# Kernel tuning notes

Measured on AMD Instinct MI355X. Metric: run time of the kernel, lower is better.

Reference implementation:

```python
import jax, jax.numpy as jnp
import numpy as np

HEADS, DIM_HEAD, BLOCK, EPS = 16, 64, 16, 1e-8


def _hattn(x, w_qkv, w_out, b_out):
    b, n, dim = x.shape
    h, dh, bsz = HEADS, DIM_HEAD, BLOCK
    scale = dh ** -0.5
    # n is a power of two, so the module's pad-to-pow2 step is a no-op.
    qkv = x @ w_qkv  # [b, n, 3*h*dh]
    q, k, v = jnp.split(qkv, 3, axis=-1)

    def to_heads(t):  # [b, n, h*dh] -> [(b h), n, dh]
        return t.reshape(b, n, h, dh).transpose(0, 2, 1, 3).reshape(b * h, n, dh)

    q, k, v = to_heads(q) * scale, to_heads(k), to_heads(v)

    num_levels = int(np.log2(n // bsz)) - 1
    levels = [(q, k, v)]
    for _ in range(num_levels):  # coarsen: mean-pool q,k; sum-pool v (mask=None path)
        q = q.reshape(b * h, -1, 2, dh).mean(axis=2)
        k = k.reshape(b * h, -1, 2, dh).mean(axis=2)
        v = v.reshape(b * h, -1, 2, dh).sum(axis=2)
        levels.append((q, k, v))

    def flip_blocks(t):  # swap adjacent blocks along the block axis: [B, nb, z, d]
        B, nb, z, d = t.shape
        return t.reshape(B, nb // 2, 2, z, d)[:, :, ::-1].reshape(B, nb, z, d)

    Ys = []
    last = len(levels) - 1
    for ind, (ql, kl, vl) in enumerate(reversed(levels)):  # coarsest -> finest
        B, N, d = ql.shape
        qb = ql.reshape(B, N // bsz, bsz, d)
        kb = vb = None
        kb = kl.reshape(B, N // bsz, bsz, d)
        vb = vl.reshape(B, N // bsz, bsz, d)
        if ind != last:  # off-diagonal pairing at coarse levels
            kb, vb = flip_blocks(kb), flip_blocks(vb)
        S = jnp.einsum('bnid,bnjd->bnij', qb, kb)
        S = S - S.max(axis=-1, keepdims=True)
        A = jnp.exp(S)
        y = jnp.einsum('bnij,bnjd->bnid', A, vb)
        Ys.append((y.reshape(B, N, d), A.sum(-1).reshape(B, N)))

    Y, Asum = Ys[0]
    for y_l, a_l in Ys[1:]:  # upsample-and-accumulate across levels
        Y = jnp.repeat(Y, 2, axis=1) + y_l
        Asum = jnp.repeat(Asum, 2, axis=1) + a_l

    out = Y / (Asum + EPS)[..., None]  # [(b h), n, dh]
    out = out.reshape(b, h, n, dh).transpose(0, 2, 1, 3).reshape(b, n, h * dh)
    return out @ w_out + b_out


def setup_inputs() -> dict:
    key = jax.random.key(0)
    k1, k2, k3 = jax.random.split(key, 3)
    b, n, dim = 4, 8192, 1024
    inner = HEADS * DIM_HEAD
    x = jax.random.normal(k1, (b, n, dim), dtype=jnp.float32)
    w_qkv = jax.random.normal(k2, (dim, inner * 3), dtype=jnp.float32) * 0.02
    w_out = jax.random.normal(k3, (inner, dim), dtype=jnp.float32) * 0.02
    b_out = jnp.zeros((dim,), dtype=jnp.float32)
    return {"x": x, "w_qkv": w_qkv, "w_out": w_out, "b_out": b_out}


def reference(x, w_qkv, w_out, b_out):
    return _hattn(x, w_qkv, w_out, b_out)
```

## Files before the change

### kernel.cpp

```cpp
#include <hip/hip_runtime.h>

typedef unsigned short u16;
typedef unsigned int u32;
typedef __bf16 bf16x8 __attribute__((ext_vector_type(8)));
typedef float f32x4 __attribute__((ext_vector_type(4)));

__device__ inline float bf2f(u16 u) { u32 x = ((u32)u) << 16; return __uint_as_float(x); }
__device__ inline u16 f2bf(float f) {
  u32 x = __float_as_uint(f);
  u32 r = (x + 0x7FFFu + ((x >> 16) & 1u)) >> 16;
  return (u16)r;
}
__device__ inline u32 pack2(float lo, float hi) {
  return (u32)f2bf(lo) | ((u32)f2bf(hi) << 16);
}

__global__ __launch_bounds__(256) void cast_bf16(const float* __restrict__ s,
                                                 u16* __restrict__ d, int n4) {
  const float4* s4 = (const float4*)s;
  u32* d2 = (u32*)d;
  int i = blockIdx.x * 256 + threadIdx.x;
  int stride = gridDim.x * 256;
  for (; i < n4; i += stride) {
    float4 f = s4[i];
    d2[2 * i]     = pack2(f.x, f.y);
    d2[2 * i + 1] = pack2(f.z, f.w);
  }
}

__global__ __launch_bounds__(256) void transpose_cast(const float* __restrict__ src,
                                                      u16* __restrict__ dst, int R, int C) {
  __shared__ float tile[32][33];
  int bx = blockIdx.x, by = blockIdx.y;
  int tx = threadIdx.x & 31, ty = threadIdx.x >> 5;
  for (int rr = ty; rr < 32; rr += 8)
    tile[rr][tx] = src[(size_t)(by * 32 + rr) * C + bx * 32 + tx];
  __syncthreads();
  for (int rr = ty; rr < 32; rr += 8)
    dst[(size_t)(bx * 32 + rr) * R + by * 32 + tx] = f2bf(tile[tx][rr]);
}

#define MFMAQ(AF, BF, MO, NO)                                                     \
  _Pragma("unroll") for (int mf = 0; mf < 4; ++mf)                                \
  _Pragma("unroll") for (int nf = 0; nf < 2; ++nf)                                \
  _Pragma("unroll") for (int kq = 0; kq < 2; ++kq)                                \
    acc[(MO) + mf][(NO) + nf] = __builtin_amdgcn_mfma_f32_16x16x32_bf16(          \
        AF[mf][kq], BF[nf][kq], acc[(MO) + mf][(NO) + nf], 0, 0, 0);

#define PH_OPEN12                                                                 \
  asm volatile("s_waitcnt lgkmcnt(8)" ::: "memory");                              \
  __builtin_amdgcn_s_barrier();                                                   \
  asm volatile("s_waitcnt lgkmcnt(0)" ::: "memory");                              \
  __builtin_amdgcn_sched_barrier(0);                                              \
  __builtin_amdgcn_s_setprio(1);

#define PH_OPEN                                                                   \
  __builtin_amdgcn_s_barrier();                                                   \
  asm volatile("s_waitcnt lgkmcnt(0)" ::: "memory");                              \
  __builtin_amdgcn_sched_barrier(0);                                              \
  __builtin_amdgcn_s_setprio(1);

#define PH_CLOSE                                                                  \
  __builtin_amdgcn_s_setprio(0);                                                  \
  __builtin_amdgcn_s_barrier();                                                   \
  __builtin_amdgcn_sched_barrier(0);

#define PH_CLOSE_VM8                                                              \
  __builtin_amdgcn_s_setprio(0);                                                  \
  asm volatile("s_waitcnt vmcnt(8)" ::: "memory");                                \
  __builtin_amdgcn_s_barrier();                                                   \
  __builtin_amdgcn_sched_barrier(0);

template <int EPI>
__global__ __launch_bounds__(512, 2) void gemm8p(
    const u16* __restrict__ A, const u16* __restrict__ Bt, int M, int N, int K, int NB,
    u16* __restrict__ q0, u16* __restrict__ k0, u16* __restrict__ v0,
    u16* __restrict__ q4, u16* __restrict__ k4, u16* __restrict__ v4,
    float* __restrict__ out, const float* __restrict__ bias) {
  __shared__ u16 ldsA[3][16384];
  __shared__ u16 ldsB[2][16384];
  const int tid = threadIdx.x;
  const int lane = tid & 63;
  const int wave = tid >> 6;
  const int wm = wave >> 2, wn = wave & 3;
  const int lr = lane & 15, lg = lane >> 4;

  const int nwg = gridDim.x;
  const int bid = blockIdx.x;
  const int swz = (bid & 7) * (nwg >> 3) + (bid >> 3);
  const int m0 = (swz / NB) * 256;
  const int n0 = (swz % NB) * 256;
  const int NT = K >> 6;

  auto stage_half = [&](u16* ldsop, const u16* src, int r0, int hb, int kt_) {
#pragma unroll
    for (int ii = 0; ii < 2; ++ii) {
      int c2 = (hb * 2 + ii) * 512 + tid;
      int row = c2 >> 3, ps = c2 & 7;
      int ks = ps ^ (row & 7);
      const u16* g = src + (size_t)(r0 + row) * K + kt_ + ks * 8;
      char* l = (char*)ldsop + (size_t)(((hb * 2 + ii) * 512 + (tid & ~63)) * 16);
      __builtin_amdgcn_global_load_lds((const __attribute__((address_space(1))) void*)g,
                                       (__attribute__((address_space(3))) void*)l, 16, 0, 0);
    }
  };
  auto rdA = [&](const u16* Ab, int mf, int kq) -> bf16x8 {
    int rl = wm * 128 + mf * 16 + lr;
    int sl = (kq * 4 + lg) ^ (rl & 7);
    return *(const bf16x8*)(Ab + rl * 64 + sl * 8);
  };
  auto rdB = [&](const u16* Bb, int nf, int kq) -> bf16x8 {
    int rl = wn * 64 + nf * 16 + lr;
    int sl = (kq * 4 + lg) ^ (rl & 7);
    return *(const bf16x8*)(Bb + rl * 64 + sl * 8);
  };

  f32x4 acc[8][4];
#pragma unroll
  for (int mf = 0; mf < 8; ++mf)
#pragma unroll
    for (int nf = 0; nf < 4; ++nf) acc[mf][nf] = f32x4{0.f, 0.f, 0.f, 0.f};

  stage_half(ldsA[0], A, m0, 0, 0); stage_half(ldsA[0], A, m0, 1, 0);
  stage_half(ldsB[0], Bt, n0, 0, 0); stage_half(ldsB[0], Bt, n0, 1, 0);
  const int k1 = ((NT > 1) ? 1 : 0) << 6;
  stage_half(ldsA[1], A, m0, 0, k1); stage_half(ldsA[1], A, m0, 1, k1);
  stage_half(ldsB[1], Bt, n0, 0, k1); stage_half(ldsB[1], Bt, n0, 1, k1);
  asm volatile("s_waitcnt vmcnt(8)" ::: "memory");
  __builtin_amdgcn_s_barrier();
  __builtin_amdgcn_sched_barrier(0);

  for (int t = 0; t < NT; ++t) {
    const u16* Ab = ldsA[t % 3];
    const u16* Bb = ldsB[t & 1];
    u16* A2 = ldsA[(t + 2) % 3];
    u16* B2 = ldsB[t & 1];
    const int k2 = (((t + 2) < NT) ? (t + 2) : (NT - 1)) << 6;

    bf16x8 afA[4][2], afB[4][2], bA[2][2], bB[2][2];
#pragma unroll
    for (int mf = 0; mf < 4; ++mf) { afA[mf][0] = rdA(Ab, mf, 0); afA[mf][1] = rdA(Ab, mf, 1); }
#pragma unroll
    for (int nf = 0; nf < 2; ++nf) { bA[nf][0] = rdB(Bb, nf, 0); bA[nf][1] = rdB(Bb, nf, 1); }
    stage_half(A2, A, m0, 0, k2);
    PH_OPEN12 MFMAQ(afA, bA, 0, 0) PH_CLOSE
#pragma unroll
    for (int nf = 0; nf < 2; ++nf) { bB[nf][0] = rdB(Bb, 2 + nf, 0); bB[nf][1] = rdB(Bb, 2 + nf, 1); }
    stage_half(A2, A, m0, 1, k2);
    PH_OPEN MFMAQ(afA, bB, 0, 2) PH_CLOSE
#pragma unroll
    for (int mf = 0; mf < 4; ++mf) { afB[mf][0] = rdA(Ab, 4 + mf, 0); afB[mf][1] = rdA(Ab, 4 + mf, 1); }
    stage_half(B2, Bt, n0, 0, k2);
    PH_OPEN MFMAQ(afB, bB, 4, 2) PH_CLOSE
    stage_half(B2, Bt, n0, 1, k2);
    PH_OPEN MFMAQ(afB, bA, 4, 0) PH_CLOSE_VM8
  }
  asm volatile("s_waitcnt vmcnt(0)" ::: "memory");

#pragma unroll
  for (int mf = 0; mf < 8; ++mf) {
#pragma unroll
    for (int nf = 0; nf < 4; ++nf) {
      int col = n0 + wn * 64 + nf * 16 + lr;
      if (EPI == 0) {
        int p = col >> 10, cc = col & 1023;
        int h = cc >> 6, d = cc & 63;
        u16* dst = (p == 0) ? q0 : (p == 1) ? k0 : v0;
        float sc = (p == 0) ? 0.125f : 1.0f;
#pragma unroll
        for (int jj = 0; jj < 4; ++jj) {
          int row = m0 + wm * 128 + mf * 16 + lg * 4 + jj;
          int b = row >> 13, nn = row & 8191;
          dst[((size_t)((b << 4) + h) * 8192 + nn) * 64 + d] = f2bf(acc[mf][nf][jj] * sc);
        }
        float s4 = acc[mf][nf][0] + acc[mf][nf][1] + acc[mf][nf][2] + acc[mf][nf][3];
        s4 += __shfl_xor(s4, 16);
        s4 += __shfl_xor(s4, 32);
        if (lane < 16) {
          int row = m0 + wm * 128 + mf * 16;
          int b = row >> 13, n4 = (row & 8191) >> 4;
          u16* dst4 = (p == 0) ? q4 : (p == 1) ? k4 : v4;
          float val = (p == 2) ? s4 : s4 * 0.0625f;
          if (p == 0) val *= 0.125f;
          dst4[((size_t)((b << 4) + h) * 512 + n4) * 64 + d] = f2bf(val);
        }
      } else {
        float bv = bias[col];
#pragma unroll
        for (int jj = 0; jj < 4; ++jj) {
          int row = m0 + wm * 128 + mf * 16 + lg * 4 + jj;
          out[(size_t)row * N + col] = acc[mf][nf][jj] + bv;
        }
      }
    }
  }
}

__global__ __launch_bounds__(256) void pool_all4(
    const u16* __restrict__ q4, const u16* __restrict__ k4, const u16* __restrict__ v4,
    u16* __restrict__ qd, u16* __restrict__ kd, u16* __restrict__ vd) {
  int t = blockIdx.x * 256 + threadIdx.x;
  if (t >= 983040) return;
  int arr = blockIdx.y;
  int col = t & 31;
  int rr = t >> 5;
  int Bi = rr / 480;
  int r = rr % 480;
  int base, w, Nl;
  if (r < 256)      { base = 0;   w = 2;  Nl = 256; }
  else if (r < 384) { base = 256; w = 4;  Nl = 128; r -= 256; }
  else if (r < 448) { base = 384; w = 8;  Nl = 64;  r -= 384; }
  else              { base = 448; w = 16; Nl = 32;  r -= 448; }
  const u32* s = (const u32*)(arr == 0 ? q4 : arr == 1 ? k4 : v4);
  const u32* src = s + ((size_t)Bi * 512 + (size_t)r * w) * 32 + col;
  float lo = 0, hi = 0;
  for (int m = 0; m < w; ++m) {
    u32 u = src[(size_t)m * 32];
    lo += bf2f((u16)u); hi += bf2f((u16)(u >> 16));
  }
  float sc = (arr == 2) ? 1.0f : (1.0f / (float)w);
  u32* d = (u32*)(arr == 0 ? qd : arr == 1 ? kd : vd);
  d[(size_t)2048 * base + ((size_t)Bi * Nl + r) * 32 + col] = pack2(lo * sc, hi * sc);
}

__global__ __launch_bounds__(256) void hattn_coarse(
    const u16* __restrict__ q4, const u16* __restrict__ k4, const u16* __restrict__ v4,
    const u16* __restrict__ qc, const u16* __restrict__ kc, const u16* __restrict__ vc,
    float* __restrict__ ylvl, float* __restrict__ alvl) {
  __shared__ float qs[16][68], ks[16][68], vs[16][68];
  __shared__ float As[16][17];
  const int bx = blockIdx.x, Bi = blockIdx.y;
  int lvl, jb;
  if (bx < 32)      { lvl = 0; jb = bx; }
  else if (bx < 48) { lvl = 1; jb = bx - 32; }
  else if (bx < 56) { lvl = 2; jb = bx - 48; }
  else if (bx < 60) { lvl = 3; jb = bx - 56; }
  else              { lvl = 4; jb = bx - 60; }
  const int N = 512 >> lvl;
  const int srcb[5] = {0, 0, 256, 384, 448};
  const int offr[5] = {0, 512, 768, 896, 960};
  const u16* qp = (lvl == 0) ? q4 : qc + (size_t)4096 * srcb[lvl];
  const u16* kp = (lvl == 0) ? k4 : kc + (size_t)4096 * srcb[lvl];
  const u16* vp = (lvl == 0) ? v4 : vc + (size_t)4096 * srcb[lvl];
  const int tid = threadIdx.x;
  const int jk = jb ^ 1;
  const u32* qg = (const u32*)(qp + ((size_t)Bi * N + jb * 16) * 64);
  const u32* kg = (const u32*)(kp + ((size_t)Bi * N + jk * 16) * 64);
  const u32* vg = (const u32*)(vp + ((size_t)Bi * N + jk * 16) * 64);
#pragma unroll
  for (int u = tid; u < 512; u += 256) {
    int row = u >> 5, dp = (u & 31) * 2;
    u32 a = qg[u]; qs[row][dp] = bf2f((u16)a); qs[row][dp + 1] = bf2f((u16)(a >> 16));
    u32 b = kg[u]; ks[row][dp] = bf2f((u16)b); ks[row][dp + 1] = bf2f((u16)(b >> 16));
    u32 c = vg[u]; vs[row][dp] = bf2f((u16)c); vs[row][dp + 1] = bf2f((u16)(c >> 16));
  }
  __syncthreads();
  const int i = tid >> 4, j = tid & 15;
  float s = 0.f;
  const float4* qv = (const float4*)&qs[i][0];
  const float4* kv = (const float4*)&ks[j][0];
#pragma unroll
  for (int d4 = 0; d4 < 16; ++d4) {
    float4 a = qv[d4], b = kv[d4];
    s += a.x * b.x + a.y * b.y + a.z * b.z + a.w * b.w;
  }
  float mx = s;
#pragma unroll
  for (int off = 8; off; off >>= 1) mx = fmaxf(mx, __shfl_xor(mx, off, 16));
  float aexp = __expf(s - mx);
  float asum = aexp;
#pragma unroll
  for (int off = 8; off; off >>= 1) asum += __shfl_xor(asum, off, 16);
  As[i][j] = aexp;
  __syncthreads();
  float y0 = 0, y1 = 0, y2 = 0, y3 = 0;
  const int d0 = j * 4;
#pragma unroll
  for (int jj = 0; jj < 16; ++jj) {
    float av = As[i][jj];
    const float4 vv = *(const float4*)&vs[jj][d0];
    y0 += av * vv.x; y1 += av * vv.y; y2 += av * vv.z; y3 += av * vv.w;
  }
  const int nf = jb * 16 + i;
  float* yo = ylvl + (size_t)4096 * offr[lvl] + ((size_t)Bi * N + nf) * 64 + d0;
  yo[0] = y0; yo[1] = y1; yo[2] = y2; yo[3] = y3;
  if (j == 0) alvl[(size_t)64 * offr[lvl] + (size_t)Bi * N + nf] = asum;
}

union F8 { u32 w[4]; bf16x8 v; };

__device__ inline void acc_row8(const u16* p, float* a) {
  const u32* qw = (const u32*)p;
#pragma unroll
  for (int m = 0; m < 4; ++m) {
    u32 u = qw[m];
    a[2 * m]     += bf2f((u16)u);
    a[2 * m + 1] += bf2f((u16)(u >> 16));
  }
}
__device__ inline bf16x8 mk8(const float* a, float s) {
  F8 f;
#pragma unroll
  for (int m = 0; m < 4; ++m) f.w[m] = pack2(a[2 * m] * s, a[2 * m + 1] * s);
  return f.v;
}
__device__ inline bf16x8 pool_frag(const u16* arr, int row0, int cnt, int slotq, float scale) {
  float a[8] = {0, 0, 0, 0, 0, 0, 0, 0};
  for (int m = 0; m < cnt; ++m) {
    int r = row0 + m;
    acc_row8(arr + r * 64 + ((slotq ^ (r & 7)) * 8), a);
  }
  return mk8(a, scale);
}
__device__ inline bf16x8 rd_frag(const u16* arr, int r, int slotq) {
  return *(const bf16x8*)(arr + r * 64 + ((slotq ^ (r & 7)) * 8));
}
template <int LVL>
__device__ inline bf16x8 vt_frag(const u16* Vt, int c, int rbase) {
  float a[8] = {0, 0, 0, 0, 0, 0, 0, 0};
  const u32* p = (const u32*)(Vt + c * 264 + rbase);
#pragma unroll
  for (int g = 0; g < (1 << LVL); ++g) {
#pragma unroll
    for (int m = 0; m < 4; ++m) {
      u32 u = p[g * 4 + m];
      int t = g * 8 + 2 * m;
      a[t >> LVL]       += bf2f((u16)u);
      a[(t + 1) >> LVL] += bf2f((u16)(u >> 16));
    }
  }
  return mk8(a, 1.0f);
}

__device__ inline bf16x8 qk_softmax(bf16x8 ka0, bf16x8 ka1, bf16x8 qb0, bf16x8 qb1,
                                    int lane, float* asum_out) {
  f32x4 s = {0.f, 0.f, 0.f, 0.f};
  s = __builtin_amdgcn_mfma_f32_16x16x32_bf16(ka0, qb0, s, 0, 0, 0);
  s = __builtin_amdgcn_mfma_f32_16x16x32_bf16(ka1, qb1, s, 0, 0, 0);
  float mx = fmaxf(fmaxf(s[0], s[1]), fmaxf(s[2], s[3]));
  mx = fmaxf(mx, __shfl_xor(mx, 32));
  mx = fmaxf(mx, __shfl_xor(mx, 16));
  float p0 = __expf(s[0] - mx), p1 = __expf(s[1] - mx);
  float p2 = __expf(s[2] - mx), p3 = __expf(s[3] - mx);
  float as = p0 + p1 + p2 + p3;
  as += __shfl_xor(as, 32);
  as += __shfl_xor(as, 16);
  *asum_out = as;
  u32 pk01 = pack2(p0, p1), pk23 = pack2(p2, p3);
  int jq = lane & 15, lg = lane >> 4;
  int a1 = ((((lg * 2) * 16) + jq) & 63) << 2;
  int a2 = ((((lg * 2 + 1) * 16) + jq) & 63) << 2;
  F8 f;
  f.w[0] = (u32)__builtin_amdgcn_ds_bpermute(a1, (int)pk01);
  f.w[1] = (u32)__builtin_amdgcn_ds_bpermute(a1, (int)pk23);
  f.w[2] = (u32)__builtin_amdgcn_ds_bpermute(a2, (int)pk01);
  f.w[3] = (u32)__builtin_amdgcn_ds_bpermute(a2, (int)pk23);
  if (lg >= 2) { f.w[0] = 0; f.w[1] = 0; f.w[2] = 0; f.w[3] = 0; }
  return f.v;
}

__global__ __launch_bounds__(512, 1) void attn_fine(
    const u16* __restrict__ q, const u16* __restrict__ k, const u16* __restrict__ v,
    const float* __restrict__ ylvl, const float* __restrict__ alvl,
    u16* __restrict__ outA) {
  __shared__ u16 Qs[16384];
  __shared__ u16 Ks[16384];
  __shared__ u16 Vt[16896];
  __shared__ float Yc1[128][68];
  __shared__ float Yc2[64][68];
  __shared__ float Yc3[32][68];
  __shared__ float SUMc[224];
  const int tid = threadIdx.x;
  const int lane = tid & 63;
  const int wv = tid >> 6;
  const int j = lane & 15, lg = lane >> 4;
  const int ci = blockIdx.x, Bi = blockIdx.y;
  const size_t gbase = ((size_t)Bi * 8192 + (size_t)ci * 256) * 64;

#pragma unroll
  for (int it = 0; it < 4; ++it) {
    int sidx = it * 512 + tid;
    int row = sidx >> 3, ps = sidx & 7;
    int ks_ = ps ^ (row & 7);
    const u16* gq = q + gbase + (size_t)row * 64 + ks_ * 8;
    const u16* gk = k + gbase + (size_t)row * 64 + ks_ * 8;
    char* lq = (char*)Qs + (size_t)(it * 512 + (tid & ~63)) * 16;
    char* lk = (char*)Ks + (size_t)(it * 512 + (tid & ~63)) * 16;
    __builtin_amdgcn_global_load_lds((const __attribute__((address_space(1))) void*)gq,
                                     (__attribute__((address_space(3))) void*)lq, 16, 0, 0);
    __builtin_amdgcn_global_load_lds((const __attribute__((address_space(1))) void*)gk,
                                     (__attribute__((address_space(3))) void*)lk, 16, 0, 0);
  }
  {
    const uint4* gv = (const uint4*)(v + gbase);
    u32* Vt32 = (u32*)Vt;
#pragma unroll
    for (int it = 0; it < 2; ++it) {
      int i = it * 512 + tid;
      int r2 = i >> 3, cg = i & 7, c0 = cg * 8;
      uint4 a = gv[(size_t)(2 * r2) * 8 + cg];
      uint4 b = gv[(size_t)(2 * r2 + 1) * 8 + cg];
      const u16* pa = (const u16*)&a;
      const u16* pb = (const u16*)&b;
#pragma unroll
      for (int m = 0; m < 8; ++m)
        Vt32[(c0 + m) * 132 + r2] = (u32)pa[m] | ((u32)pb[m] << 16);
    }
  }
  __syncthreads();

  {
    int kb = wv ^ 1;
    bf16x8 ka0 = pool_frag(Ks, kb * 32 + 2 * j, 2, lg, 0.5f);
    bf16x8 ka1 = pool_frag(Ks, kb * 32 + 2 * j, 2, 4 + lg, 0.5f);
    bf16x8 qb0 = pool_frag(Qs, wv * 32 + 2 * j, 2, lg, 0.5f);
    bf16x8 qb1 = pool_frag(Qs, wv * 32 + 2 * j, 2, 4 + lg, 0.5f);
    float as;
    bf16x8 pa = qk_softmax(ka0, ka1, qb0, qb1, lane, &as);
    if (lg == 0) SUMc[wv * 16 + j] = as;
    int rb = kb * 32 + (lg & 1) * 16;
    f32x4 acc[4];
#pragma unroll
    for (int ch = 0; ch < 4; ++ch) {
      bf16x8 vb = vt_frag<1>(Vt, ch * 16 + j, rb);
      acc[ch] = __builtin_amdgcn_mfma_f32_16x16x32_bf16(pa, vb, f32x4{0.f,0.f,0.f,0.f}, 0, 0, 0);
    }
#pragma unroll
    for (int ch = 0; ch < 4; ++ch)
#pragma unroll
      for (int jj = 0; jj < 4; ++jj)
        Yc1[wv * 16 + lg * 4 + jj][ch * 16 + j] = acc[ch][jj];
  }
  if (wv < 4) {
    int kb = wv ^ 1;
    bf16x8 ka0 = pool_frag(Ks, kb * 64 + 4 * j, 4, lg, 0.25f);
    bf16x8 ka1 = pool_frag(Ks, kb * 64 + 4 * j, 4, 4 + lg, 0.25f);
    bf16x8 qb0 = pool_frag(Qs, wv * 64 + 4 * j, 4, lg, 0.25f);
    bf16x8 qb1 = pool_frag(Qs, wv * 64 + 4 * j, 4, 4 + lg, 0.25f);
    float as;
    bf16x8 pa = qk_softmax(ka0, ka1, qb0, qb1, lane, &as);
    if (lg == 0) SUMc[128 + wv * 16 + j] = as;
    int rb = kb * 64 + (lg & 1) * 32;
    f32x4 acc[4];
#pragma unroll
    for (int ch = 0; ch < 4; ++ch) {
      bf16x8 vb = vt_frag<2>(Vt, ch * 16 + j, rb);
      acc[ch] = __builtin_amdgcn_mfma_f32_16x16x32_bf16(pa, vb, f32x4{0.f,0.f,0.f,0.f}, 0, 0, 0);
    }
#pragma unroll
    for (int ch = 0; ch < 4; ++ch)
#pragma unroll
      for (int jj = 0; jj < 4; ++jj)
        Yc2[wv * 16 + lg * 4 + jj][ch * 16 + j] = acc[ch][jj];
  }
  if (wv >= 6) {
    int w3 = wv - 6;
    int kb = w3 ^ 1;
    bf16x8 ka0 = pool_frag(Ks, kb * 128 + 8 * j, 8, lg, 0.125f);
    bf16x8 ka1 = pool_frag(Ks, kb * 128 + 8 * j, 8, 4 + lg, 0.125f);
    bf16x8 qb0 = pool_frag(Qs, w3 * 128 + 8 * j, 8, lg, 0.125f);
    bf16x8 qb1 = pool_frag(Qs, w3 * 128 + 8 * j, 8, 4 + lg, 0.125f);
    float as;
    bf16x8 pa = qk_softmax(ka0, ka1, qb0, qb1, lane, &as);
    if (lg == 0) SUMc[192 + w3 * 16 + j] = as;
    int rb = kb * 128 + (lg & 1) * 64;
    f32x4 acc[4];
#pragma unroll
    for (int ch = 0; ch < 4; ++ch) {
      bf16x8 vb = vt_frag<3>(Vt, ch * 16 + j, rb);
      acc[ch] = __builtin_amdgcn_mfma_f32_16x16x32_bf16(pa, vb, f32x4{0.f,0.f,0.f,0.f}, 0, 0, 0);
    }
#pragma unroll
    for (int ch = 0; ch < 4; ++ch)
#pragma unroll
      for (int jj = 0; jj < 4; ++jj)
        Yc3[w3 * 16 + lg * 4 + jj][ch * 16 + j] = acc[ch][jj];
  }
  __syncthreads();

  const int batch = Bi >> 4, h = Bi & 15;
  const int offr[5] = {0, 512, 768, 896, 960};
#pragma unroll
  for (int bb = 0; bb < 2; ++bb) {
    int b = wv * 2 + bb;
    bf16x8 ka0 = rd_frag(Ks, b * 16 + j, lg);
    bf16x8 ka1 = rd_frag(Ks, b * 16 + j, 4 + lg);
    bf16x8 qb0 = rd_frag(Qs, b * 16 + j, lg);
    bf16x8 qb1 = rd_frag(Qs, b * 16 + j, 4 + lg);
    float as;
    bf16x8 pa = qk_softmax(ka0, ka1, qb0, qb1, lane, &as);
    float av[4];
#pragma unroll
    for (int jj = 0; jj < 4; ++jj)
      av[jj] = __int_as_float(__builtin_amdgcn_ds_bpermute((lg * 4 + jj) << 2,
                                                           __float_as_int(as)));
    int rb = b * 16 + (lg & 1) * 8;
    f32x4 acc[4];
#pragma unroll
    for (int ch = 0; ch < 4; ++ch) {
      bf16x8 vb = *(const bf16x8*)(Vt + (ch * 16 + j) * 264 + rb);
      acc[ch] = __builtin_amdgcn_mfma_f32_16x16x32_bf16(pa, vb, f32x4{0.f,0.f,0.f,0.f}, 0, 0, 0);
    }
    const int i4 = ci * 16 + b;
    float a4 = 0;
    float y4v[4] = {0, 0, 0, 0};
#pragma unroll
    for (int l = 0; l < 5; ++l) {
      int Rl = 512 >> l;
      size_t idx = (size_t)Bi * Rl + (i4 >> l);
      a4 += alvl[(size_t)64 * offr[l] + idx];
      const float* yp = ylvl + (size_t)4096 * offr[l] + idx * 64;
#pragma unroll
      for (int ch = 0; ch < 4; ++ch) y4v[ch] += yp[ch * 16 + j];
    }
#pragma unroll
    for (int jj = 0; jj < 4; ++jj) {
      int r0 = b * 16 + lg * 4 + jj;
      float at = av[jj] + SUMc[r0 >> 1] + SUMc[128 + (r0 >> 2)] + SUMc[192 + (r0 >> 3)] + a4;
      float inv = 1.0f / (at + 1e-8f);
      size_t n = (size_t)ci * 256 + r0;
      u16* orow = outA + ((size_t)batch * 8192 + n) * 1024 + h * 64 + j;
#pragma unroll
      for (int ch = 0; ch < 4; ++ch) {
        float yt = acc[ch][jj] + Yc1[r0 >> 1][ch * 16 + j] + Yc2[r0 >> 2][ch * 16 + j] +
                   Yc3[r0 >> 3][ch * 16 + j] + y4v[ch];
        orow[ch * 16] = f2bf(yt * inv);
      }
    }
  }
}

extern "C" void kernel_launch(void* const* d_in, const int* in_sizes, int n_in,
                              void* d_out, int out_size, void* d_ws, size_t ws_size,
                              hipStream_t stream) {
  const float* x = (const float*)d_in[0];
  const float* w_qkv = (const float*)d_in[1];
  const float* w_out = (const float*)d_in[2];
  const float* b_out = (const float*)d_in[3];
  float* out = (float*)d_out;

  char* ws = (char*)d_ws;
  size_t off = 0;
  auto alloc = [&](size_t bytes) -> char* {
    char* p = ws + off;
    off += (bytes + 255) & ~(size_t)255;
    return p;
  };
  u16* xb = (u16*)alloc(33554432ull * 2);
  u16* wqkvT = (u16*)alloc(3072ull * 1024 * 2);
  u16* woutT = (u16*)alloc(1024ull * 1024 * 2);
  u16* q0 = (u16*)alloc(67108864ull);
  u16* k0 = (u16*)alloc(67108864ull);
  u16* v0 = (u16*)alloc(67108864ull);
  u16* q4 = (u16*)alloc(4194304ull);
  u16* k4 = (u16*)alloc(4194304ull);
  u16* v4 = (u16*)alloc(4194304ull);
  u16* qc = (u16*)alloc(3932160ull);
  u16* kc = (u16*)alloc(3932160ull);
  u16* vc = (u16*)alloc(3932160ull);
  float* ylvl = (float*)alloc(16252928ull);
  float* alvl = (float*)alloc(253952ull);
  (void)ws_size; (void)in_sizes; (void)n_in; (void)out_size;

  cast_bf16<<<2048, 256, 0, stream>>>(x, xb, 33554432 / 4);
  transpose_cast<<<dim3(3072 / 32, 1024 / 32), 256, 0, stream>>>(w_qkv, wqkvT, 1024, 3072);
  transpose_cast<<<dim3(1024 / 32, 1024 / 32), 256, 0, stream>>>(w_out, woutT, 1024, 1024);

  gemm8p<0><<<1536, 512, 0, stream>>>(xb, wqkvT, 32768, 3072, 1024, 12,
                                      q0, k0, v0, q4, k4, v4, nullptr, nullptr);

  pool_all4<<<dim3(3840, 3), 256, 0, stream>>>(q4, k4, v4, qc, kc, vc);
  hattn_coarse<<<dim3(62, 64), 256, 0, stream>>>(q4, k4, v4, qc, kc, vc, ylvl, alvl);
  attn_fine<<<dim3(32, 64), 512, 0, stream>>>(q0, k0, v0, ylvl, alvl, xb);

  gemm8p<1><<<512, 512, 0, stream>>>(xb, woutT, 32768, 1024, 1024, 4,
                                     nullptr, nullptr, nullptr,
                                     nullptr, nullptr, nullptr, out, b_out);
}
```

Baseline: 495.5 us.

## Restructure GEMM LDS pipeline to two double buffers with unrolled even/odd iterations

Replaces the triple-buffered A / double-buffered B LDS layout with a uniform 2x2 buffer array and unrolls the K loop by two. Buffer indices become compile-time constants, so the modulo-3 addressing goes away. The issue order of the prefetch stages and the vmcnt wait threshold change so A and B tiles rotate between two buffers. This cuts LDS use from 160KB to 128KB and simplifies addressing. In exchange the prefetch distance shrinks for A and the code assumes NT is even.

```diff
diff --git a/kernel.cpp b/kernel.cpp
--- a/kernel.cpp
+++ b/kernel.cpp
@@ -65,9 +65,9 @@
   __builtin_amdgcn_s_barrier();                                                   \
   __builtin_amdgcn_sched_barrier(0);
 
-#define PH_CLOSE_VM8                                                              \
+#define PH_CLOSE_VM                                                               \
   __builtin_amdgcn_s_setprio(0);                                                  \
-  asm volatile("s_waitcnt vmcnt(8)" ::: "memory");                                \
+  asm volatile("s_waitcnt vmcnt(4)" ::: "memory");                                \
   __builtin_amdgcn_s_barrier();                                                   \
   __builtin_amdgcn_sched_barrier(0);
 
@@ -77,8 +77,7 @@
     u16* __restrict__ q0, u16* __restrict__ k0, u16* __restrict__ v0,
     u16* __restrict__ q4, u16* __restrict__ k4, u16* __restrict__ v4,
     float* __restrict__ out, const float* __restrict__ bias) {
-  __shared__ u16 ldsA[3][16384];
-  __shared__ u16 ldsB[2][16384];
+  __shared__ u16 lds[2][2][16384];
   const int tid = threadIdx.x;
   const int lane = tid & 63;
   const int wave = tid >> 6;
@@ -91,28 +90,32 @@
   const int m0 = (swz / NB) * 256;
   const int n0 = (swz % NB) * 256;
   const int NT = K >> 6;
-
-  auto stage_half = [&](u16* ldsop, const u16* src, int r0, int hb, int kt_) {
+  const int NI = NT >> 1;
+
+  auto stage_half = [&](int buf, int ht, int kt_) {
+    const u16* src = (ht < 2) ? A : Bt;
+    const int r0 = (ht < 2) ? m0 : n0;
+    u16* ldsop = &lds[buf][ht >> 1][0];
 #pragma unroll
     for (int ii = 0; ii < 2; ++ii) {
-      int c2 = (hb * 2 + ii) * 512 + tid;
+      int c2 = ((ht & 1) * 2 + ii) * 512 + tid;
       int row = c2 >> 3, ps = c2 & 7;
       int ks = ps ^ (row & 7);
       const u16* g = src + (size_t)(r0 + row) * K + kt_ + ks * 8;
-      char* l = (char*)ldsop + (size_t)(((hb * 2 + ii) * 512 + (tid & ~63)) * 16);
+      char* l = (char*)ldsop + (size_t)((((ht & 1) * 2 + ii) * 512 + (tid & ~63)) * 16);
       __builtin_amdgcn_global_load_lds((const __attribute__((address_space(1))) void*)g,
                                        (__attribute__((address_space(3))) void*)l, 16, 0, 0);
     }
   };
-  auto rdA = [&](const u16* Ab, int mf, int kq) -> bf16x8 {
+  auto rdA = [&](int c, int mf, int kq) -> bf16x8 {
     int rl = wm * 128 + mf * 16 + lr;
     int sl = (kq * 4 + lg) ^ (rl & 7);
-    return *(const bf16x8*)(Ab + rl * 64 + sl * 8);
+    return *(const bf16x8*)(&lds[c][0][rl * 64 + sl * 8]);
   };
-  auto rdB = [&](const u16* Bb, int nf, int kq) -> bf16x8 {
+  auto rdB = [&](int c, int nf, int kq) -> bf16x8 {
     int rl = wn * 64 + nf * 16 + lr;
     int sl = (kq * 4 + lg) ^ (rl & 7);
-    return *(const bf16x8*)(Bb + rl * 64 + sl * 8);
+    return *(const bf16x8*)(&lds[c][1][rl * 64 + sl * 8]);
   };
 
   f32x4 acc[8][4];
@@ -121,39 +124,51 @@
 #pragma unroll
     for (int nf = 0; nf < 4; ++nf) acc[mf][nf] = f32x4{0.f, 0.f, 0.f, 0.f};
 
-  stage_half(ldsA[0], A, m0, 0, 0); stage_half(ldsA[0], A, m0, 1, 0);
-  stage_half(ldsB[0], Bt, n0, 0, 0); stage_half(ldsB[0], Bt, n0, 1, 0);
-  const int k1 = ((NT > 1) ? 1 : 0) << 6;
-  stage_half(ldsA[1], A, m0, 0, k1); stage_half(ldsA[1], A, m0, 1, k1);
-  stage_half(ldsB[1], Bt, n0, 0, k1); stage_half(ldsB[1], Bt, n0, 1, k1);
-  asm volatile("s_waitcnt vmcnt(8)" ::: "memory");
+  stage_half(0, 2, 0); stage_half(0, 3, 0); stage_half(0, 0, 0); stage_half(0, 1, 0);
+  stage_half(1, 2, 64); stage_half(1, 3, 64);
+  asm volatile("s_waitcnt vmcnt(4)" ::: "memory");
   __builtin_amdgcn_s_barrier();
   __builtin_amdgcn_sched_barrier(0);
 
-  for (int t = 0; t < NT; ++t) {
-    const u16* Ab = ldsA[t % 3];
-    const u16* Bb = ldsB[t & 1];
-    u16* A2 = ldsA[(t + 2) % 3];
-    u16* B2 = ldsB[t & 1];
-    const int k2 = (((t + 2) < NT) ? (t + 2) : (NT - 1)) << 6;
-
-    bf16x8 afA[4][2], afB[4][2], bA[2][2], bB[2][2];
-#pragma unroll
-    for (int mf = 0; mf < 4; ++mf) { afA[mf][0] = rdA(Ab, mf, 0); afA[mf][1] = rdA(Ab, mf, 1); }
-#pragma unroll
-    for (int nf = 0; nf < 2; ++nf) { bA[nf][0] = rdB(Bb, nf, 0); bA[nf][1] = rdB(Bb, nf, 1); }
-    stage_half(A2, A, m0, 0, k2);
+  bf16x8 afA[4][2], afB[4][2], bA[2][2], bB[2][2];
+  for (int it = 0; it < NI; ++it) {
+    const int kO  = (2 * it + 1) << 6;
+    const int t2  = 2 * it + 2, t3 = 2 * it + 3;
+    const int kE2 = ((t2 < NT) ? t2 : NT - 1) << 6;
+    const int kO2 = ((t3 < NT) ? t3 : NT - 1) << 6;
+
+#pragma unroll
+    for (int mf = 0; mf < 4; ++mf) { afA[mf][0] = rdA(0, mf, 0); afA[mf][1] = rdA(0, mf, 1); }
+#pragma unroll
+    for (int nf = 0; nf < 2; ++nf) { bA[nf][0] = rdB(0, nf, 0); bA[nf][1] = rdB(0, nf, 1); }
+    stage_half(1, 0, kO);
     PH_OPEN12 MFMAQ(afA, bA, 0, 0) PH_CLOSE
 #pragma unroll
-    for (int nf = 0; nf < 2; ++nf) { bB[nf][0] = rdB(Bb, 2 + nf, 0); bB[nf][1] = rdB(Bb, 2 + nf, 1); }
-    stage_half(A2, A, m0, 1, k2);
+    for (int nf = 0; nf < 2; ++nf) { bB[nf][0] = rdB(0, 2 + nf, 0); bB[nf][1] = rdB(0, 2 + nf, 1); }
+    stage_half(1, 1, kO);
     PH_OPEN MFMAQ(afA, bB, 0, 2) PH_CLOSE
 #pragma unroll
-    for (int mf = 0; mf < 4; ++mf) { afB[mf][0] = rdA(Ab, 4 + mf, 0); afB[mf][1] = rdA(Ab, 4 + mf, 1); }
-    stage_half(B2, Bt, n0, 0, k2);
+    for (int mf = 0; mf < 4; ++mf) { afB[mf][0] = rdA(0, 4 + mf, 0); afB[mf][1] = rdA(0, 4 + mf, 1); }
+    stage_half(0, 2, kE2);
     PH_OPEN MFMAQ(afB, bB, 4, 2) PH_CLOSE
-    stage_half(B2, Bt, n0, 1, k2);
-    PH_OPEN MFMAQ(afB, bA, 4, 0) PH_CLOSE_VM8
+    stage_half(0, 3, kE2);
+    PH_OPEN MFMAQ(afB, bA, 4, 0) PH_CLOSE_VM
+#pragma unroll
+    for (int mf = 0; mf < 4; ++mf) { afA[mf][0] = rdA(1, mf, 0); afA[mf][1] = rdA(1, mf, 1); }
+#pragma unroll
+    for (int nf = 0; nf < 2; ++nf) { bA[nf][0] = rdB(1, nf, 0); bA[nf][1] = rdB(1, nf, 1); }
+    stage_half(0, 0, kE2);
+    PH_OPEN12 MFMAQ(afA, bA, 0, 0) PH_CLOSE
+#pragma unroll
+    for (int nf = 0; nf < 2; ++nf) { bB[nf][0] = rdB(1, 2 + nf, 0); bB[nf][1] = rdB(1, 2 + nf, 1); }
+    stage_half(0, 1, kE2);
+    PH_OPEN MFMAQ(afA, bB, 0, 2) PH_CLOSE
+#pragma unroll
+    for (int mf = 0; mf < 4; ++mf) { afB[mf][0] = rdA(1, 4 + mf, 0); afB[mf][1] = rdA(1, 4 + mf, 1); }
+    stage_half(1, 2, kO2);
+    PH_OPEN MFMAQ(afB, bB, 4, 2) PH_CLOSE
+    stage_half(1, 3, kO2);
+    PH_OPEN MFMAQ(afB, bA, 4, 0) PH_CLOSE_VM
   }
   asm volatile("s_waitcnt vmcnt(0)" ::: "memory");
 
```

New measurement: 469.5 us. 5.2% less time.

## Restructure GEMM pipeline into K-half LDS units with finer-grained prefetch

Applied to the files above, without the earlier changes.

The GEMM's LDS staging changes from a triple-buffered A and double-buffered B on 64-wide K tiles to double buffers split into two 32-wide K halves per operand. Each loop phase now loads four A and four B fragments and issues a full 4x4 MFMA block, with prefetch of the next K half interleaved between phases. A new XOR swizzle matches the 32-element row stride. The aim is better overlap of global-to-LDS loads with MFMA and fewer fragment registers, in exchange for more barriers per K tile and tighter timing on the vmcnt waits.

```diff
diff --git a/kernel.cpp b/kernel.cpp
--- a/kernel.cpp
+++ b/kernel.cpp
@@ -40,19 +40,11 @@
     dst[(size_t)(bx * 32 + rr) * R + by * 32 + tx] = f2bf(tile[tx][rr]);
 }
 
-#define MFMAQ(AF, BF, MO, NO)                                                     \
+#define MFMAK(AF, BF, MO)                                                         \
   _Pragma("unroll") for (int mf = 0; mf < 4; ++mf)                                \
-  _Pragma("unroll") for (int nf = 0; nf < 2; ++nf)                                \
-  _Pragma("unroll") for (int kq = 0; kq < 2; ++kq)                                \
-    acc[(MO) + mf][(NO) + nf] = __builtin_amdgcn_mfma_f32_16x16x32_bf16(          \
-        AF[mf][kq], BF[nf][kq], acc[(MO) + mf][(NO) + nf], 0, 0, 0);
-
-#define PH_OPEN12                                                                 \
-  asm volatile("s_waitcnt lgkmcnt(8)" ::: "memory");                              \
-  __builtin_amdgcn_s_barrier();                                                   \
-  asm volatile("s_waitcnt lgkmcnt(0)" ::: "memory");                              \
-  __builtin_amdgcn_sched_barrier(0);                                              \
-  __builtin_amdgcn_s_setprio(1);
+  _Pragma("unroll") for (int nf = 0; nf < 4; ++nf)                                \
+    acc[(MO) + mf][nf] = __builtin_amdgcn_mfma_f32_16x16x32_bf16(                 \
+        AF[mf], BF[nf], acc[(MO) + mf][nf], 0, 0, 0);
 
 #define PH_OPEN                                                                   \
   __builtin_amdgcn_s_barrier();                                                   \
@@ -72,13 +64,13 @@
   __builtin_amdgcn_sched_barrier(0);
 
 template <int EPI>
-__global__ __launch_bounds__(512, 2) void gemm8p(
+__global__ __launch_bounds__(512, 2) void gemmk(
     const u16* __restrict__ A, const u16* __restrict__ Bt, int M, int N, int K, int NB,
     u16* __restrict__ q0, u16* __restrict__ k0, u16* __restrict__ v0,
     u16* __restrict__ q4, u16* __restrict__ k4, u16* __restrict__ v4,
     float* __restrict__ out, const float* __restrict__ bias) {
-  __shared__ u16 ldsA[3][16384];
-  __shared__ u16 ldsB[2][16384];
+  __shared__ u16 ldsA[2][2][8192];
+  __shared__ u16 ldsB[2][2][8192];
   const int tid = threadIdx.x;
   const int lane = tid & 63;
   const int wave = tid >> 6;
@@ -91,28 +83,33 @@
   const int m0 = (swz / NB) * 256;
   const int n0 = (swz % NB) * 256;
   const int NT = K >> 6;
-
-  auto stage_half = [&](u16* ldsop, const u16* src, int r0, int hb, int kt_) {
+  (void)M;
+
+  auto stage_unit = [&](int opB, int buf, int kh, int kt_) {
+    const u16* src = opB ? Bt : A;
+    const int r0 = opB ? n0 : m0;
+    u16* dstb = opB ? &ldsB[buf][kh][0] : &ldsA[buf][kh][0];
 #pragma unroll
     for (int ii = 0; ii < 2; ++ii) {
-      int c2 = (hb * 2 + ii) * 512 + tid;
-      int row = c2 >> 3, ps = c2 & 7;
-      int ks = ps ^ (row & 7);
-      const u16* g = src + (size_t)(r0 + row) * K + kt_ + ks * 8;
-      char* l = (char*)ldsop + (size_t)(((hb * 2 + ii) * 512 + (tid & ~63)) * 16);
+      int e = ii * 4096 + tid * 8;
+      int row = e >> 5;
+      int ps = (e >> 3) & 3;
+      int ks = ps ^ ((row >> 1) & 3);
+      const u16* g = src + (size_t)(r0 + row) * K + kt_ + kh * 32 + ks * 8;
+      char* l = (char*)dstb + ii * 8192 + (size_t)(tid & ~63) * 16;
       __builtin_amdgcn_global_load_lds((const __attribute__((address_space(1))) void*)g,
                                        (__attribute__((address_space(3))) void*)l, 16, 0, 0);
     }
   };
-  auto rdA = [&](const u16* Ab, int mf, int kq) -> bf16x8 {
+  auto rdA = [&](int buf, int kh, int mf) -> bf16x8 {
     int rl = wm * 128 + mf * 16 + lr;
-    int sl = (kq * 4 + lg) ^ (rl & 7);
-    return *(const bf16x8*)(Ab + rl * 64 + sl * 8);
+    int sl = lg ^ ((rl >> 1) & 3);
+    return *(const bf16x8*)(&ldsA[buf][kh][rl * 32 + sl * 8]);
   };
-  auto rdB = [&](const u16* Bb, int nf, int kq) -> bf16x8 {
+  auto rdB = [&](int buf, int kh, int nf) -> bf16x8 {
     int rl = wn * 64 + nf * 16 + lr;
-    int sl = (kq * 4 + lg) ^ (rl & 7);
-    return *(const bf16x8*)(Bb + rl * 64 + sl * 8);
+    int sl = lg ^ ((rl >> 1) & 3);
+    return *(const bf16x8*)(&ldsB[buf][kh][rl * 32 + sl * 8]);
   };
 
   f32x4 acc[8][4];
@@ -121,39 +118,42 @@
 #pragma unroll
     for (int nf = 0; nf < 4; ++nf) acc[mf][nf] = f32x4{0.f, 0.f, 0.f, 0.f};
 
-  stage_half(ldsA[0], A, m0, 0, 0); stage_half(ldsA[0], A, m0, 1, 0);
-  stage_half(ldsB[0], Bt, n0, 0, 0); stage_half(ldsB[0], Bt, n0, 1, 0);
-  const int k1 = ((NT > 1) ? 1 : 0) << 6;
-  stage_half(ldsA[1], A, m0, 0, k1); stage_half(ldsA[1], A, m0, 1, k1);
-  stage_half(ldsB[1], Bt, n0, 0, k1); stage_half(ldsB[1], Bt, n0, 1, k1);
+  const int k1t = ((NT > 1) ? 1 : 0) << 6;
+  stage_unit(0, 0, 0, 0);
+  stage_unit(1, 0, 0, 0);
+  stage_unit(0, 0, 1, 0);
+  stage_unit(1, 0, 1, 0);
+  stage_unit(0, 1, 0, k1t);
+  stage_unit(1, 1, 0, k1t);
   asm volatile("s_waitcnt vmcnt(8)" ::: "memory");
   __builtin_amdgcn_s_barrier();
   __builtin_amdgcn_sched_barrier(0);
 
   for (int t = 0; t < NT; ++t) {
-    const u16* Ab = ldsA[t % 3];
-    const u16* Bb = ldsB[t & 1];
-    u16* A2 = ldsA[(t + 2) % 3];
-    u16* B2 = ldsB[t & 1];
-    const int k2 = (((t + 2) < NT) ? (t + 2) : (NT - 1)) << 6;
-
-    bf16x8 afA[4][2], afB[4][2], bA[2][2], bB[2][2];
-#pragma unroll
-    for (int mf = 0; mf < 4; ++mf) { afA[mf][0] = rdA(Ab, mf, 0); afA[mf][1] = rdA(Ab, mf, 1); }
-#pragma unroll
-    for (int nf = 0; nf < 2; ++nf) { bA[nf][0] = rdB(Bb, nf, 0); bA[nf][1] = rdB(Bb, nf, 1); }
-    stage_half(A2, A, m0, 0, k2);
-    PH_OPEN12 MFMAQ(afA, bA, 0, 0) PH_CLOSE
-#pragma unroll
-    for (int nf = 0; nf < 2; ++nf) { bB[nf][0] = rdB(Bb, 2 + nf, 0); bB[nf][1] = rdB(Bb, 2 + nf, 1); }
-    stage_half(A2, A, m0, 1, k2);
-    PH_OPEN MFMAQ(afA, bB, 0, 2) PH_CLOSE
-#pragma unroll
-    for (int mf = 0; mf < 4; ++mf) { afB[mf][0] = rdA(Ab, 4 + mf, 0); afB[mf][1] = rdA(Ab, 4 + mf, 1); }
-    stage_half(B2, Bt, n0, 0, k2);
-    PH_OPEN MFMAQ(afB, bB, 4, 2) PH_CLOSE
-    stage_half(B2, Bt, n0, 1, k2);
-    PH_OPEN MFMAQ(afB, bA, 4, 0) PH_CLOSE_VM8
+    const int c = t & 1;
+    const int kA = (((t + 1) < NT) ? (t + 1) : (NT - 1)) << 6;
+    const int kB = (((t + 2) < NT) ? (t + 2) : (NT - 1)) << 6;
+    bf16x8 af[4], bfr[4];
+#pragma unroll
+    for (int mf = 0; mf < 4; ++mf) af[mf] = rdA(c, 0, mf);
+#pragma unroll
+    for (int nf = 0; nf < 4; ++nf) bfr[nf] = rdB(c, 0, nf);
+    stage_unit(0, c ^ 1, 1, kA);
+    PH_OPEN MFMAK(af, bfr, 0) PH_CLOSE
+#pragma unroll
+    for (int mf = 0; mf < 4; ++mf) af[mf] = rdA(c, 0, 4 + mf);
+    stage_unit(1, c ^ 1, 1, kA);
+    PH_OPEN MFMAK(af, bfr, 4) PH_CLOSE_VM8
+#pragma unroll
+    for (int mf = 0; mf < 4; ++mf) af[mf] = rdA(c, 1, mf);
+#pragma unroll
+    for (int nf = 0; nf < 4; ++nf) bfr[nf] = rdB(c, 1, nf);
+    stage_unit(0, c, 0, kB);
+    PH_OPEN MFMAK(af, bfr, 0) PH_CLOSE
+#pragma unroll
+    for (int mf = 0; mf < 4; ++mf) af[mf] = rdA(c, 1, 4 + mf);
+    stage_unit(1, c, 0, kB);
+    PH_OPEN MFMAK(af, bfr, 4) PH_CLOSE_VM8
   }
   asm volatile("s_waitcnt vmcnt(0)" ::: "memory");
 
@@ -566,14 +566,14 @@
   transpose_cast<<<dim3(3072 / 32, 1024 / 32), 256, 0, stream>>>(w_qkv, wqkvT, 1024, 3072);
   transpose_cast<<<dim3(1024 / 32, 1024 / 32), 256, 0, stream>>>(w_out, woutT, 1024, 1024);
 
-  gemm8p<0><<<1536, 512, 0, stream>>>(xb, wqkvT, 32768, 3072, 1024, 12,
-                                      q0, k0, v0, q4, k4, v4, nullptr, nullptr);
+  gemmk<0><<<1536, 512, 0, stream>>>(xb, wqkvT, 32768, 3072, 1024, 12,
+                                     q0, k0, v0, q4, k4, v4, nullptr, nullptr);
 
   pool_all4<<<dim3(3840, 3), 256, 0, stream>>>(q4, k4, v4, qc, kc, vc);
   hattn_coarse<<<dim3(62, 64), 256, 0, stream>>>(q4, k4, v4, qc, kc, vc, ylvl, alvl);
   attn_fine<<<dim3(32, 64), 512, 0, stream>>>(q0, k0, v0, ylvl, alvl, xb);
 
-  gemm8p<1><<<512, 512, 0, stream>>>(xb, woutT, 32768, 1024, 1024, 4,
-                                     nullptr, nullptr, nullptr,
-                                     nullptr, nullptr, nullptr, out, b_out);
-}
+  gemmk<1><<<512, 512, 0, stream>>>(xb, woutT, 32768, 1024, 1024, 4,
+                                    nullptr, nullptr, nullptr,
+                                    nullptr, nullptr, nullptr, out, b_out);
+}
```

After: 557.2 us. 12.5% more time.
